# Kernel tuning notes

Hardware: AMD Instinct MI355X
Metric: run time of the kernel (lower is better)

Reference implementation:

```python
import jax, jax.numpy as jnp
import numpy as np

V, D, N, K = 500000, 64, 50000, 32


def setup_inputs() -> dict:
    key = jax.random.key(0)
    ks = jax.random.split(key, 8)
    return {
        "embeddings": jax.random.normal(ks[0], (V, D), dtype=jnp.float32),
        "W1": jax.random.normal(ks[1], (2 * D, D), dtype=jnp.float32) * 0.05,
        "b1": jnp.zeros((D,), dtype=jnp.float32),
        "W2": jax.random.normal(ks[2], (D, D), dtype=jnp.float32) * 0.05,
        "b2": jnp.zeros((D,), dtype=jnp.float32),
        "w3": jax.random.normal(ks[3], (D, 1), dtype=jnp.float32) * 0.05,
        "b3": jnp.zeros((1,), dtype=jnp.float32),
        "video_nodes": jax.random.randint(ks[4], (N,), 0, V, dtype=jnp.int32),
        "neigh_idx": jax.random.randint(ks[5], (N, K), 0, V, dtype=jnp.int32),
        "neigh_deg": jax.random.randint(ks[6], (N,), 0, K + 1, dtype=jnp.int32),
    }


def reference(embeddings, W1, b1, W2, b2, w3, b3, video_nodes, neigh_idx, neigh_deg):
    # Ragged neighbor gather (padded to K, masked by degree)
    e = embeddings[neigh_idx]                      # [N, K, D] neighbor embeddings
    u = embeddings[video_nodes]                    # [N, D]    center embeddings
    # GraphRec-style attention: MLP on [neigh, center] concat -> scalar score
    x = jnp.concatenate(
        [e, jnp.broadcast_to(u[:, None, :], e.shape)], axis=-1)  # [N, K, 2D]
    h = jax.nn.relu(x @ W1 + b1)
    h = jax.nn.relu(h @ W2 + b2)
    s = (h @ w3)[..., 0] + b3[0]                   # [N, K]
    mask = jnp.arange(K)[None, :] < neigh_deg[:, None]
    s = jnp.where(mask, s, -1e9)                   # mask padded neighbors
    att = jax.nn.softmax(s, axis=-1)               # softmax over valid neighbors
    out = jnp.einsum('nkd,nk->nd', e, att)         # attention-weighted sum
    # num_neighs == 0 -> fall back to node's own embedding
    out = jnp.where((neigh_deg > 0)[:, None], out, u)
    return out
```

## Files before the change

### kernel.cpp

```cpp
#include <hip/hip_runtime.h>
#include <hip/hip_bf16.h>

typedef __bf16 bf16x8 __attribute__((ext_vector_type(8)));
typedef float  f32x4  __attribute__((ext_vector_type(4)));

#define MFMA32(acc, a, b) acc = __builtin_amdgcn_mfma_f32_16x16x32_bf16(a, b, acc, 0, 0, 0)

__device__ __forceinline__ bf16x8 cvt8(float4 a, float4 b) {
  bf16x8 r;
  r[0] = (__bf16)a.x; r[1] = (__bf16)a.y; r[2] = (__bf16)a.z; r[3] = (__bf16)a.w;
  r[4] = (__bf16)b.x; r[5] = (__bf16)b.y; r[6] = (__bf16)b.z; r[7] = (__bf16)b.w;
  return r;
}

__global__ void prep_frags(const float* __restrict__ W1,
                           const float* __restrict__ W2,
                           __bf16* __restrict__ wf) {
  int idx = blockIdx.x * 256 + threadIdx.x;
  if (idx < 8192) {
    int j = idx & 7, lane = (idx >> 3) & 63, mt = (idx >> 9) & 3, ks = idx >> 11;
    int i = ks * 32 + ((lane >> 4) << 3) + j;
    int col = mt * 16 + (lane & 15);
    wf[idx] = (__bf16)W1[i * 64 + col];
  } else if (idx < 12288) {
    int t = idx - 8192;
    int j = t & 7, lane = (t >> 3) & 63, mt2 = (t >> 9) & 3, ks2 = (t >> 11) & 1;
    int g = (lane >> 4) & 3;
    int rho = (ks2 * 2 + (j >> 2)) * 16 + g * 4 + (j & 3);
    wf[idx] = (__bf16)W2[rho * 64 + mt2 * 16 + (lane & 15)];
  }
}

__global__ __launch_bounds__(256, 4) void graph_agg(
    const float* __restrict__ emb,
    const float* __restrict__ b1g,
    const float* __restrict__ b2g,
    const float* __restrict__ w3g,
    const float* __restrict__ b3g,
    const int* __restrict__ vn,
    const int* __restrict__ ni,
    const int* __restrict__ nd,
    const __bf16* __restrict__ wf,
    float* __restrict__ out,
    int N) {
  __shared__ __align__(16) unsigned char smem[25344];

  {
    const uint4* src = (const uint4*)wf;
    uint4* dst = (uint4*)smem;
#pragma unroll
    for (int i = 0; i < 6; i++) dst[threadIdx.x + i * 256] = src[threadIdx.x + i * 256];
    int t = threadIdx.x;
    if (t < 64) {
      ((float*)(smem + 24576))[t] = b1g[t];
      ((float*)(smem + 24832))[t] = b2g[t];
      ((float*)(smem + 25088))[t] = w3g[t];
    }
  }
  __syncthreads();

  const __bf16* w1f = (const __bf16*)smem;
  const __bf16* w2f = (const __bf16*)(smem + 16384);
  const int wid = threadIdx.x >> 6;
  const int l   = threadIdx.x & 63;
  const int g   = l >> 4;
  const int lr  = l & 15;
  const float b3v = b3g[0];

  const int gw = blockIdx.x * 4 + wid;
  const int nwaves = gridDim.x * 4;

  int n = gw;
  int node = 0, deg = 0, i0 = 0, i1 = 0;
  if (n < N) {
    node = vn[n]; deg = nd[n];
    i0 = ni[n * 32 + lr]; i1 = ni[n * 32 + 16 + lr];
  }

  for (; n < N; n += nwaves) {
    const int cn = node, cd = deg, ci0 = i0, ci1 = i1;
    {
      int nn = n + nwaves; if (nn >= N) nn = n;
      node = vn[nn]; deg = nd[nn];
      i0 = ni[nn * 32 + lr]; i1 = ni[nn * 32 + 16 + lr];
    }
    const float* ub = emb + (long)cn * 64;

    if (cd == 0) {
      out[(long)n * 64 + l] = ub[l];
      continue;
    }
    const bool m1 = (cd > 16);

    int boff = 24576;
    asm volatile("" : "+v"(boff));
    const unsigned char* bb = smem + boff;

    bf16x8 ef[2][2];
    bf16x8 uf[2];
    {
      const bool v = (lr < cd);
      const float* p = emb + (long)(v ? ci0 : cn) * 64 + g * 8;
      float4 a0 = *(const float4*)p,        a1 = *(const float4*)(p + 4);
      float4 c0 = *(const float4*)(p + 32), c1 = *(const float4*)(p + 36);
      if (!v) { a0 = a1 = c0 = c1 = make_float4(0.f, 0.f, 0.f, 0.f); }
      ef[0][0] = cvt8(a0, a1); ef[0][1] = cvt8(c0, c1);
    }
    if (m1) {
      const bool v = (16 + lr < cd);
      const float* p = emb + (long)(v ? ci1 : cn) * 64 + g * 8;
      float4 a0 = *(const float4*)p,        a1 = *(const float4*)(p + 4);
      float4 c0 = *(const float4*)(p + 32), c1 = *(const float4*)(p + 36);
      if (!v) { a0 = a1 = c0 = c1 = make_float4(0.f, 0.f, 0.f, 0.f); }
      ef[1][0] = cvt8(a0, a1); ef[1][1] = cvt8(c0, c1);
    }
    {
      const float* q = ub + g * 8;
      uf[0] = cvt8(*(const float4*)q,        *(const float4*)(q + 4));
      uf[1] = cvt8(*(const float4*)(q + 32), *(const float4*)(q + 36));
    }

    f32x4 acc1[4][2];
#pragma unroll
    for (int mt = 0; mt < 4; mt++) {
      f32x4 bv = *(const f32x4*)(bb + (mt * 16 + g * 4) * 4);
      acc1[mt][0] = bv; acc1[mt][1] = bv;
    }
#pragma unroll
    for (int ks = 0; ks < 4; ks++) {
      bf16x8 xb0 = (ks < 2) ? ef[0][ks] : uf[ks - 2];
#pragma unroll
      for (int mt = 0; mt < 4; mt++) {
        bf16x8 wa = *(const bf16x8*)(w1f + ((ks * 4 + mt) * 64 + l) * 8);
        MFMA32(acc1[mt][0], wa, xb0);
        if (m1) {
          bf16x8 xb1 = (ks < 2) ? ef[1][ks] : uf[ks - 2];
          MFMA32(acc1[mt][1], wa, xb1);
        }
      }
    }

    bf16x8 hb[2][2];
#pragma unroll
    for (int ks2 = 0; ks2 < 2; ks2++) {
#pragma unroll
      for (int nt = 0; nt < 2; nt++) {
        if (nt == 0 || m1) {
          bf16x8 v;
#pragma unroll
          for (int j = 0; j < 8; j++) {
            const int mt = ks2 * 2 + (j >> 2), r = j & 3;
            v[j] = (__bf16)fmaxf(acc1[mt][nt][r], 0.f);
          }
          hb[ks2][nt] = v;
        }
      }
    }

    f32x4 acc2[4][2];
#pragma unroll
    for (int mt2 = 0; mt2 < 4; mt2++) {
      f32x4 bv = *(const f32x4*)(bb + 256 + (mt2 * 16 + g * 4) * 4);
      acc2[mt2][0] = bv; acc2[mt2][1] = bv;
    }
#pragma unroll
    for (int ks2 = 0; ks2 < 2; ks2++) {
#pragma unroll
      for (int mt2 = 0; mt2 < 4; mt2++) {
        bf16x8 wa = *(const bf16x8*)(w2f + ((ks2 * 4 + mt2) * 64 + l) * 8);
        MFMA32(acc2[mt2][0], wa, hb[ks2][0]);
        if (m1) MFMA32(acc2[mt2][1], wa, hb[ks2][1]);
      }
    }

    float sv0 = 0.f, sv1 = 0.f;
    {
#pragma unroll
      for (int mt2 = 0; mt2 < 4; mt2++) {
        f32x4 wv = *(const f32x4*)(bb + 512 + (mt2 * 16 + g * 4) * 4);
#pragma unroll
        for (int r = 0; r < 4; r++) {
          sv0 += fmaxf(acc2[mt2][0][r], 0.f) * wv[r];
          if (m1) sv1 += fmaxf(acc2[mt2][1][r], 0.f) * wv[r];
        }
      }
    }
    sv0 += __shfl_xor(sv0, 16); sv0 += __shfl_xor(sv0, 32);
    if (m1) { sv1 += __shfl_xor(sv1, 16); sv1 += __shfl_xor(sv1, 32); }

    const bool v0 = (lr < cd);
    const bool v1 = m1 && (16 + lr < cd);
    sv0 = v0 ? (sv0 + b3v) : -1e30f;
    sv1 = v1 ? (sv1 + b3v) : -1e30f;

    float mx = fmaxf(sv0, sv1);
    mx = fmaxf(mx, __shfl_xor(mx, 1));
    mx = fmaxf(mx, __shfl_xor(mx, 2));
    mx = fmaxf(mx, __shfl_xor(mx, 4));
    mx = fmaxf(mx, __shfl_xor(mx, 8));

    float p0 = v0 ? __expf(sv0 - mx) : 0.f;
    float p1 = v1 ? __expf(sv1 - mx) : 0.f;
    float sum = p0 + p1;
    sum += __shfl_xor(sum, 1);
    sum += __shfl_xor(sum, 2);
    sum += __shfl_xor(sum, 4);
    sum += __shfl_xor(sum, 8);
    const float inv = 1.f / sum;
    const float a0 = p0 * inv, a1 = p1 * inv;

    float o[16];
#pragma unroll
    for (int ks = 0; ks < 2; ks++)
#pragma unroll
      for (int j = 0; j < 8; j++) {
        float v = a0 * (float)ef[0][ks][j];
        if (m1) v += a1 * (float)ef[1][ks][j];
        o[ks * 8 + j] = v;
      }
#pragma unroll
    for (int mask = 1; mask < 16; mask <<= 1)
#pragma unroll
      for (int t = 0; t < 16; t++) o[t] += __shfl_xor(o[t], mask);

    if (lr == 0) {
      float* op = out + (long)n * 64;
      *(float4*)(op + g * 8)      = make_float4(o[0],  o[1],  o[2],  o[3]);
      *(float4*)(op + g * 8 + 4)  = make_float4(o[4],  o[5],  o[6],  o[7]);
      *(float4*)(op + 32 + g * 8) = make_float4(o[8],  o[9],  o[10], o[11]);
      *(float4*)(op + 36 + g * 8) = make_float4(o[12], o[13], o[14], o[15]);
    }
  }
}

extern "C" void kernel_launch(void* const* d_in, const int* in_sizes, int n_in,
                              void* d_out, int out_size, void* d_ws, size_t ws_size,
                              hipStream_t stream) {
  const float* emb = (const float*)d_in[0];
  const float* W1  = (const float*)d_in[1];
  const float* b1  = (const float*)d_in[2];
  const float* W2  = (const float*)d_in[3];
  const float* b2  = (const float*)d_in[4];
  const float* w3  = (const float*)d_in[5];
  const float* b3  = (const float*)d_in[6];
  const int* vn = (const int*)d_in[7];
  const int* ni = (const int*)d_in[8];
  const int* nd = (const int*)d_in[9];
  float* out = (float*)d_out;
  const int N = in_sizes[7];
  __bf16* wf = (__bf16*)d_ws;

  prep_frags<<<48, 256, 0, stream>>>(W1, W2, wf);
  graph_agg<<<1536, 256, 0, stream>>>(emb, b1, b2, w3, b3, vn, ni, nd, wf, out, N);
}
```

Before: 86.02 us.

## Use DPP cross-lane reductions and enlarge blocks to 512 threads

Replaces the ds_swizzle/bpermute-based __shfl_xor reductions for the softmax max/sum and the output aggregation with DPP row operations. The output reduction now uses row_shr, which accumulates the full row sum in lane 15, so that lane does the store. Blocks grow to 512 threads (8 waves) with launch bounds allowing 8 blocks per CU, and the grid shrinks to 1024 blocks, so the shared-memory weight copy is amortised over more waves. The tighter launch bound may force register limits and cause spills.

```diff
diff --git a/kernel.cpp b/kernel.cpp
--- a/kernel.cpp
+++ b/kernel.cpp
@@ -11,6 +11,17 @@
   r[0] = (__bf16)a.x; r[1] = (__bf16)a.y; r[2] = (__bf16)a.z; r[3] = (__bf16)a.w;
   r[4] = (__bf16)b.x; r[5] = (__bf16)b.y; r[6] = (__bf16)b.z; r[7] = (__bf16)b.w;
   return r;
+}
+
+template <int CTRL>
+__device__ __forceinline__ float dpp_fadd(float x) {
+  int yi = __builtin_amdgcn_update_dpp(0, __builtin_bit_cast(int, x), CTRL, 0xF, 0xF, true);
+  return x + __builtin_bit_cast(float, yi);
+}
+template <int CTRL>
+__device__ __forceinline__ float dpp_fmax(float x) {
+  int yi = __builtin_amdgcn_update_dpp(0, __builtin_bit_cast(int, x), CTRL, 0xF, 0xF, true);
+  return fmaxf(x, __builtin_bit_cast(float, yi));
 }
 
 __global__ void prep_frags(const float* __restrict__ W1,
@@ -31,7 +42,7 @@
   }
 }
 
-__global__ __launch_bounds__(256, 4) void graph_agg(
+__global__ __launch_bounds__(512, 8) void graph_agg(
     const float* __restrict__ emb,
     const float* __restrict__ b1g,
     const float* __restrict__ b2g,
@@ -49,7 +60,7 @@
     const uint4* src = (const uint4*)wf;
     uint4* dst = (uint4*)smem;
 #pragma unroll
-    for (int i = 0; i < 6; i++) dst[threadIdx.x + i * 256] = src[threadIdx.x + i * 256];
+    for (int i = 0; i < 3; i++) dst[threadIdx.x + i * 512] = src[threadIdx.x + i * 512];
     int t = threadIdx.x;
     if (t < 64) {
       ((float*)(smem + 24576))[t] = b1g[t];
@@ -67,8 +78,8 @@
   const int lr  = l & 15;
   const float b3v = b3g[0];
 
-  const int gw = blockIdx.x * 4 + wid;
-  const int nwaves = gridDim.x * 4;
+  const int gw = blockIdx.x * 8 + wid;
+  const int nwaves = gridDim.x * 8;
 
   int n = gw;
   int node = 0, deg = 0, i0 = 0, i1 = 0;
@@ -194,18 +205,18 @@
     sv1 = v1 ? (sv1 + b3v) : -1e30f;
 
     float mx = fmaxf(sv0, sv1);
-    mx = fmaxf(mx, __shfl_xor(mx, 1));
-    mx = fmaxf(mx, __shfl_xor(mx, 2));
-    mx = fmaxf(mx, __shfl_xor(mx, 4));
-    mx = fmaxf(mx, __shfl_xor(mx, 8));
+    mx = dpp_fmax<0x128>(mx);
+    mx = dpp_fmax<0x124>(mx);
+    mx = dpp_fmax<0x122>(mx);
+    mx = dpp_fmax<0x121>(mx);
 
     float p0 = v0 ? __expf(sv0 - mx) : 0.f;
     float p1 = v1 ? __expf(sv1 - mx) : 0.f;
     float sum = p0 + p1;
-    sum += __shfl_xor(sum, 1);
-    sum += __shfl_xor(sum, 2);
-    sum += __shfl_xor(sum, 4);
-    sum += __shfl_xor(sum, 8);
+    sum = dpp_fadd<0x128>(sum);
+    sum = dpp_fadd<0x124>(sum);
+    sum = dpp_fadd<0x122>(sum);
+    sum = dpp_fadd<0x121>(sum);
     const float inv = 1.f / sum;
     const float a0 = p0 * inv, a1 = p1 * inv;
 
@@ -219,11 +230,14 @@
         o[ks * 8 + j] = v;
       }
 #pragma unroll
-    for (int mask = 1; mask < 16; mask <<= 1)
-#pragma unroll
-      for (int t = 0; t < 16; t++) o[t] += __shfl_xor(o[t], mask);
-
-    if (lr == 0) {
+    for (int t = 0; t < 16; t++) {
+      o[t] = dpp_fadd<0x118>(o[t]);
+      o[t] = dpp_fadd<0x114>(o[t]);
+      o[t] = dpp_fadd<0x112>(o[t]);
+      o[t] = dpp_fadd<0x111>(o[t]);
+    }
+
+    if (lr == 15) {
       float* op = out + (long)n * 64;
       *(float4*)(op + g * 8)      = make_float4(o[0],  o[1],  o[2],  o[3]);
       *(float4*)(op + g * 8 + 4)  = make_float4(o[4],  o[5],  o[6],  o[7]);
@@ -251,5 +265,5 @@
   __bf16* wf = (__bf16*)d_ws;
 
   prep_frags<<<48, 256, 0, stream>>>(W1, W2, wf);
-  graph_agg<<<1536, 256, 0, stream>>>(emb, b1, b2, w3, b3, vn, ni, nd, wf, out, N);
-}
+  graph_agg<<<1024, 512, 0, stream>>>(emb, b1, b2, w3, b3, vn, ni, nd, wf, out, N);
+}
```

After: 187.4 us. 2.18x slower.
